# Performance work log

Hardware: AMD Instinct MI355X
Metric: run time of the kernel (lower is better)

Reference implementation:

```python
import jax, jax.numpy as jnp
import numpy as np

KL_W = 1.0
RECON_W = 1.0
TEMP_W = 0.1


def setup_inputs() -> dict:
    key = jax.random.key(0)
    ks = jax.random.split(key, 6)
    B, S, N, D = 4, 10, 2048, 128
    return {
        "pred_points": jax.random.normal(ks[0], (B, S, N, 3), jnp.float32),
        "target_points": jax.random.normal(ks[1], (B, S, N, 3), jnp.float32),
        "prior_mean": jax.random.normal(ks[2], (B, S, D), jnp.float32),
        "prior_log_var": jax.random.normal(ks[3], (B, S, D), jnp.float32),
        "posterior_mean": jax.random.normal(ks[4], (B, S, D), jnp.float32),
        "posterior_log_var": jax.random.normal(ks[5], (B, S, D), jnp.float32),
    }


def _chamfer(pred, tgt):
    # pred, tgt: [B, S, N, 3]; scan over time to keep only one [B,N,N] tile live
    B, S = pred.shape[0], pred.shape[1]

    def step(acc, pt):
        p, g = pt  # each [B, N, 3]
        diff = p[:, :, None, :] - g[:, None, :, :]            # [B, N, N, 3]
        d = jnp.sqrt(jnp.sum(diff * diff, axis=-1))           # [B, N, N]
        cd = jnp.mean(jnp.min(d, axis=2), axis=1) + jnp.mean(jnp.min(d, axis=1), axis=1)
        return acc + cd, None

    init = jnp.zeros((B,), pred.dtype)
    total, _ = jax.lax.scan(step, init,
                            (jnp.swapaxes(pred, 0, 1), jnp.swapaxes(tgt, 0, 1)))
    return jnp.mean(total) / S  # reduction='mean'


def _kl(prior_mean, prior_log_var, post_mean, post_log_var):
    kl = 0.5 * jnp.sum(
        prior_log_var - post_log_var
        + (jnp.exp(post_log_var) + (post_mean - prior_mean) ** 2) / jnp.exp(prior_log_var)
        - 1.0,
        axis=-1,
    )
    return jnp.mean(kl)


def _temporal(pred):
    diff = pred[:, 1:] - pred[:, :-1]                         # [B, S-1, N, 3]
    return jnp.mean(jnp.sqrt(jnp.sum(diff * diff, axis=-1)))


def reference(pred_points, target_points, prior_mean, prior_log_var,
              posterior_mean, posterior_log_var):
    recon = _chamfer(pred_points, target_points)
    kl = _kl(prior_mean, prior_log_var, posterior_mean, posterior_log_var)
    temporal = _temporal(pred_points)
    uncertainty = jnp.asarray(0.0, pred_points.dtype)
    total = RECON_W * recon + KL_W * kl + TEMP_W * temporal + 0.1 * uncertainty
    return (total, recon, kl, temporal, uncertainty)
```

## Files before the change

kernel.cpp:

```cpp
#include <hip/hip_runtime.h>
#include <hip/hip_bf16.h>
#include <math.h>

constexpr int B = 4, S = 10, N = 2048, D = 128;

constexpr int THREADS = 256;
constexpr int GHALF   = 1024;
constexpr int QBLK    = 256;
constexpr int QW      = 64;
constexpr int GT      = GHALF / 16;
constexpr int CHAM_BLOCKS = B * S * 2 * 2 * (N / QBLK);
constexpr int TOTQ    = B * S * 2 * N;
constexpr int TEMP_ELEMS = B * (S - 1) * N;
constexpr int TEMP_BLOCKS = 16;
constexpr int TEMP_PER_BLOCK = TEMP_ELEMS / TEMP_BLOCKS;
constexpr int KL_ELEMS = B * S * D;
constexpr int K2_BLOCKS = TOTQ / THREADS;
constexpr int K2_GRID   = K2_BLOCKS + TEMP_BLOCKS + 1;

constexpr size_t WS_SMAX  = 0;
constexpr size_t WS_CHSUM = (size_t)2 * TOTQ;
constexpr size_t WS_TPART = WS_CHSUM + K2_BLOCKS;
constexpr size_t WS_KL    = WS_TPART + TEMP_BLOCKS;

typedef __attribute__((ext_vector_type(8))) short bf16x8;
typedef __attribute__((ext_vector_type(4))) float f32x4;

__device__ __forceinline__ unsigned short f2bf(float f) {
    unsigned int b = __float_as_uint(f);
    b += 0x7FFFu + ((b >> 16) & 1u);
    return (unsigned short)(b >> 16);
}
__device__ __forceinline__ float bf2f(unsigned short h) {
    return __uint_as_float(((unsigned int)h) << 16);
}

__device__ __forceinline__ float block_sum(float v, float* red) {
    #pragma unroll
    for (int off = 32; off > 0; off >>= 1)
        v += __shfl_down(v, off, 64);
    const int wid = threadIdx.x >> 6;
    if ((threadIdx.x & 63) == 0) red[wid] = v;
    __syncthreads();
    return red[0] + red[1] + red[2] + red[3];
}

__global__ __launch_bounds__(256) void k1_kernel(
        const float* __restrict__ pred, const float* __restrict__ tgt,
        float* __restrict__ ws) {
    __shared__ alignas(16) unsigned short ghm[GT][16][8];
    __shared__ alignas(16) unsigned short glm[GT][16][8];
    __shared__ alignas(16) unsigned short zbuf[8];

    const int bid = blockIdx.x;
    const int tid = threadIdx.x;
    const int qg  = bid & 7;
    const int gh  = (bid >> 3) & 1;
    const int dir = (bid >> 4) & 1;
    const int bs  = bid >> 5;
    const float* qb  = (dir ? tgt : pred) + (size_t)bs * N * 3;
    const float* dbp = (dir ? pred : tgt) + (size_t)bs * N * 3;

    if (tid < 8) zbuf[tid] = 0;

    #pragma unroll
    for (int k = 0; k < 4; ++k) {
        const int p  = tid + 256 * k;
        const int gp = gh * GHALF + p;
        const float x = dbp[3 * gp + 0];
        const float y = dbp[3 * gp + 1];
        const float z = dbp[3 * gp + 2];
        const unsigned short hx = f2bf(x), hy = f2bf(y), hz = f2bf(z);
        const unsigned short lx = f2bf(x - bf2f(hx));
        const unsigned short ly = f2bf(y - bf2f(hy));
        const unsigned short lz = f2bf(z - bf2f(hz));
        const float m  = -0.5f * (x * x + y * y + z * z);
        const unsigned short mh = f2bf(m);
        const float m1 = m - bf2f(mh);
        const unsigned short ml = f2bf(m1);
        const unsigned short m3 = f2bf(m1 - bf2f(ml));
        bf16x8 gv, lv;
        gv[0] = (short)hx; gv[1] = (short)hy; gv[2] = (short)hz;
        gv[3] = (short)hx; gv[4] = (short)hy; gv[5] = (short)hz;
        gv[6] = (short)mh; gv[7] = (short)ml;
        lv[0] = (short)lx; lv[1] = (short)ly; lv[2] = (short)lz;
        lv[3] = (short)m3; lv[4] = 0; lv[5] = 0; lv[6] = 0; lv[7] = 0;
        *(bf16x8*)&ghm[p >> 4][p & 15][0] = gv;
        *(bf16x8*)&glm[p >> 4][p & 15][0] = lv;
    }

    const int lane = tid & 63, wid = tid >> 6;
    const int hi = lane >> 4, r = lane & 15;
    const int qwave = qg * QBLK + wid * QW;
    const short ONE = (short)0x3F80;
    bf16x8 a[4];
    #pragma unroll
    for (int qi = 0; qi < 4; ++qi) {
        bf16x8 v = (bf16x8)0;
        if (hi < 2) {
            const int q = qwave + qi * 16 + r;
            const float x = qb[3 * q + 0], y = qb[3 * q + 1], z = qb[3 * q + 2];
            const unsigned short hx = f2bf(x), hy = f2bf(y), hz = f2bf(z);
            if (hi == 0) {
                v[0] = (short)hx; v[1] = (short)hy; v[2] = (short)hz;
                v[3] = (short)f2bf(x - bf2f(hx));
                v[4] = (short)f2bf(y - bf2f(hy));
                v[5] = (short)f2bf(z - bf2f(hz));
                v[6] = ONE; v[7] = 0;
            } else {
                v[0] = (short)hx; v[1] = (short)hy; v[2] = (short)hz;
                v[3] = ONE;
            }
        }
        a[qi] = v;
    }
    __syncthreads();

    const char* bbase = (hi == 0) ? (const char*)&ghm[0][r][0]
                      : (hi == 1) ? (const char*)&glm[0][r][0]
                      :             (const char*)&zbuf[0];
    const int bstride = (hi < 2) ? 256 : 0;

    f32x4 rmax[4];
    #pragma unroll
    for (int qi = 0; qi < 4; ++qi) rmax[qi] = (f32x4)(-1e30f);
    const f32x4 zero4 = (f32x4)0.0f;

    for (int tp = 0; tp < GT / 2; ++tp) {
        const bf16x8 b0 = *(const bf16x8*)(bbase + (2 * tp + 0) * bstride);
        const bf16x8 b1 = *(const bf16x8*)(bbase + (2 * tp + 1) * bstride);
        #pragma unroll
        for (int qi = 0; qi < 4; ++qi) {
            const f32x4 c0 = __builtin_amdgcn_mfma_f32_16x16x32_bf16(a[qi], b0, zero4, 0, 0, 0);
            const f32x4 c1 = __builtin_amdgcn_mfma_f32_16x16x32_bf16(a[qi], b1, zero4, 0, 0, 0);
            #pragma unroll
            for (int j = 0; j < 4; ++j)
                rmax[qi][j] = fmaxf(rmax[qi][j], fmaxf(c0[j], c1[j]));
        }
    }

    #pragma unroll
    for (int qi = 0; qi < 4; ++qi) {
        #pragma unroll
        for (int j = 0; j < 4; ++j) {
            float v = rmax[qi][j];
            v = fmaxf(v, __shfl_xor(v, 1, 64));
            v = fmaxf(v, __shfl_xor(v, 2, 64));
            v = fmaxf(v, __shfl_xor(v, 4, 64));
            v = fmaxf(v, __shfl_xor(v, 8, 64));
            rmax[qi][j] = v;
        }
    }
    if (r == 0) {
        float* base = ws + WS_SMAX + (size_t)gh * TOTQ
                    + (size_t)(bs * 2 + dir) * N + qwave;
        #pragma unroll
        for (int qi = 0; qi < 4; ++qi)
            #pragma unroll
            for (int j = 0; j < 4; ++j)
                base[qi * 16 + hi * 4 + j] = rmax[qi][j];
    }
}

__global__ __launch_bounds__(256) void k2_kernel(
        const float* __restrict__ pred, const float* __restrict__ tgt,
        const float* __restrict__ prior_mean, const float* __restrict__ prior_lv,
        const float* __restrict__ post_mean,  const float* __restrict__ post_lv,
        float* __restrict__ ws) {
    __shared__ float red[4];
    const int bid = blockIdx.x;
    const int tid = threadIdx.x;

    if (bid < K2_BLOCKS) {
        const int u = bid * THREADS + tid;
        const float s = fmaxf(ws[WS_SMAX + u], ws[WS_SMAX + TOTQ + u]);
        const int n   = u & (N - 1);
        const int bsd = u >> 11;
        const int dir = bsd & 1, bs = bsd >> 1;
        const float* q = (dir ? tgt : pred) + ((size_t)bs * N + n) * 3;
        const float x = q[0], y = q[1], z = q[2];
        const float pn = x * x + y * y + z * z;
        const float d = sqrtf(fmaxf(pn - 2.0f * s, 0.0f));
        const float tot = block_sum(d, red);
        if (tid == 0) ws[WS_CHSUM + bid] = tot;
    } else if (bid < K2_BLOCKS + TEMP_BLOCKS) {
        const int tb = bid - K2_BLOCKS;
        float s = 0.0f;
        for (int it = 0; it < TEMP_PER_BLOCK / THREADS; ++it) {
            const int i = tb * TEMP_PER_BLOCK + it * THREADS + tid;
            const int b = i / ((S - 1) * N);
            const int rr = i % ((S - 1) * N);
            const float* p0 = pred + (size_t)(b * S * N + rr) * 3;
            const float* p1 = p0 + (size_t)N * 3;
            const float dx = p1[0] - p0[0];
            const float dy = p1[1] - p0[1];
            const float dz = p1[2] - p0[2];
            s += sqrtf(dx * dx + dy * dy + dz * dz);
        }
        const float tot = block_sum(s, red);
        if (tid == 0) ws[WS_TPART + tb] = tot;
    } else {
        float s = 0.0f;
        for (int it = 0; it < KL_ELEMS / THREADS; ++it) {
            const int i = it * THREADS + tid;
            const float aa = prior_lv[i];
            const float bb = post_lv[i];
            const float dm = post_mean[i] - prior_mean[i];
            s += aa - bb + (expf(bb) + dm * dm) * expf(-aa) - 1.0f;
        }
        const float tot = block_sum(s, red);
        if (tid == 0) ws[WS_KL] = tot;
    }
}

__global__ __launch_bounds__(256) void k3_kernel(const float* __restrict__ ws,
                                                 float* __restrict__ out) {
    __shared__ float red[4];
    float s = 0.0f;
    for (int i = threadIdx.x; i < K2_BLOCKS; i += THREADS)
        s += ws[WS_CHSUM + i];
    const float tot = block_sum(s, red);
    if (threadIdx.x == 0) {
        float tsum = 0.0f;
        for (int i = 0; i < TEMP_BLOCKS; ++i) tsum += ws[WS_TPART + i];
        const float recon    = tot / (float)(B * S * N);
        const float kl       = 0.5f * ws[WS_KL] / (float)(B * S);
        const float temporal = tsum / (float)TEMP_ELEMS;
        out[0] = recon + kl + 0.1f * temporal;
        out[1] = recon;
        out[2] = kl;
        out[3] = temporal;
        out[4] = 0.0f;
    }
}

extern "C" void kernel_launch(void* const* d_in, const int* in_sizes, int n_in,
                              void* d_out, int out_size, void* d_ws, size_t ws_size,
                              hipStream_t stream) {
    const float* pred = (const float*)d_in[0];
    const float* tgt  = (const float*)d_in[1];
    const float* pm   = (const float*)d_in[2];
    const float* plv  = (const float*)d_in[3];
    const float* qm   = (const float*)d_in[4];
    const float* qlv  = (const float*)d_in[5];
    float* out = (float*)d_out;
    float* ws  = (float*)d_ws;

    k1_kernel<<<CHAM_BLOCKS, THREADS, 0, stream>>>(pred, tgt, ws);
    k2_kernel<<<K2_GRID, THREADS, 0, stream>>>(pred, tgt, pm, plv, qm, qlv, ws);
    k3_kernel<<<1, THREADS, 0, stream>>>(ws, out);
}
```

Measured before the change: 97.69 us.

## Use 32x32 MFMA over full gallery and fuse chamfer finalize with temporal/KL

Each chamfer block now holds the full 2048-point gallery in LDS, uses 512 threads, and runs a 32x32x16 bf16 MFMA so the gallery no longer has to be split in halves. The min-distance finalize, temporal term and KL term move into the same kernel. This removes one launch and the workspace round-trip of partial maxima. In exchange LDS use and accumulator register pressure grow and the grid has half as many blocks.

```diff
diff --git a/kernel.cpp b/kernel.cpp
--- a/kernel.cpp
+++ b/kernel.cpp
@@ -4,27 +4,23 @@
 
 constexpr int B = 4, S = 10, N = 2048, D = 128;
 
-constexpr int THREADS = 256;
-constexpr int GHALF   = 1024;
+constexpr int THREADS = 512;
 constexpr int QBLK    = 256;
-constexpr int QW      = 64;
-constexpr int GT      = GHALF / 16;
-constexpr int CHAM_BLOCKS = B * S * 2 * 2 * (N / QBLK);
-constexpr int TOTQ    = B * S * 2 * N;
+constexpr int NQG     = N / QBLK;
+constexpr int GT      = N / 32;
+constexpr int CHAM_BLOCKS = B * S * 2 * NQG;
 constexpr int TEMP_ELEMS = B * (S - 1) * N;
 constexpr int TEMP_BLOCKS = 16;
 constexpr int TEMP_PER_BLOCK = TEMP_ELEMS / TEMP_BLOCKS;
 constexpr int KL_ELEMS = B * S * D;
-constexpr int K2_BLOCKS = TOTQ / THREADS;
-constexpr int K2_GRID   = K2_BLOCKS + TEMP_BLOCKS + 1;
-
-constexpr size_t WS_SMAX  = 0;
-constexpr size_t WS_CHSUM = (size_t)2 * TOTQ;
-constexpr size_t WS_TPART = WS_CHSUM + K2_BLOCKS;
+constexpr int K1_GRID  = CHAM_BLOCKS + TEMP_BLOCKS + 1;
+
+constexpr size_t WS_CHSUM = 0;
+constexpr size_t WS_TPART = CHAM_BLOCKS;
 constexpr size_t WS_KL    = WS_TPART + TEMP_BLOCKS;
 
-typedef __attribute__((ext_vector_type(8))) short bf16x8;
-typedef __attribute__((ext_vector_type(4))) float f32x4;
+typedef __attribute__((ext_vector_type(8)))  short bf16x8;
+typedef __attribute__((ext_vector_type(16))) float f32x16;
 
 __device__ __forceinline__ unsigned short f2bf(float f) {
     unsigned int b = __float_as_uint(f);
@@ -42,149 +38,121 @@
     const int wid = threadIdx.x >> 6;
     if ((threadIdx.x & 63) == 0) red[wid] = v;
     __syncthreads();
-    return red[0] + red[1] + red[2] + red[3];
-}
-
-__global__ __launch_bounds__(256) void k1_kernel(
+    float s = 0.0f;
+    if (threadIdx.x == 0)
+        #pragma unroll
+        for (int w = 0; w < 8; ++w) s += red[w];
+    return s;
+}
+
+__global__ __launch_bounds__(512) void k1_kernel(
         const float* __restrict__ pred, const float* __restrict__ tgt,
+        const float* __restrict__ prior_mean, const float* __restrict__ prior_lv,
+        const float* __restrict__ post_mean,  const float* __restrict__ post_lv,
         float* __restrict__ ws) {
-    __shared__ alignas(16) unsigned short ghm[GT][16][8];
-    __shared__ alignas(16) unsigned short glm[GT][16][8];
-    __shared__ alignas(16) unsigned short zbuf[8];
+    __shared__ alignas(16) unsigned short bh[GT][32][8];
+    __shared__ alignas(16) unsigned short bl[GT][32][8];
+    __shared__ float sm[8][32];
+    __shared__ float red[8];
 
     const int bid = blockIdx.x;
     const int tid = threadIdx.x;
-    const int qg  = bid & 7;
-    const int gh  = (bid >> 3) & 1;
-    const int dir = (bid >> 4) & 1;
-    const int bs  = bid >> 5;
-    const float* qb  = (dir ? tgt : pred) + (size_t)bs * N * 3;
-    const float* dbp = (dir ? pred : tgt) + (size_t)bs * N * 3;
-
-    if (tid < 8) zbuf[tid] = 0;
-
-    #pragma unroll
-    for (int k = 0; k < 4; ++k) {
-        const int p  = tid + 256 * k;
-        const int gp = gh * GHALF + p;
-        const float x = dbp[3 * gp + 0];
-        const float y = dbp[3 * gp + 1];
-        const float z = dbp[3 * gp + 2];
-        const unsigned short hx = f2bf(x), hy = f2bf(y), hz = f2bf(z);
-        const unsigned short lx = f2bf(x - bf2f(hx));
-        const unsigned short ly = f2bf(y - bf2f(hy));
-        const unsigned short lz = f2bf(z - bf2f(hz));
-        const float m  = -0.5f * (x * x + y * y + z * z);
-        const unsigned short mh = f2bf(m);
-        const float m1 = m - bf2f(mh);
-        const unsigned short ml = f2bf(m1);
-        const unsigned short m3 = f2bf(m1 - bf2f(ml));
-        bf16x8 gv, lv;
-        gv[0] = (short)hx; gv[1] = (short)hy; gv[2] = (short)hz;
-        gv[3] = (short)hx; gv[4] = (short)hy; gv[5] = (short)hz;
-        gv[6] = (short)mh; gv[7] = (short)ml;
-        lv[0] = (short)lx; lv[1] = (short)ly; lv[2] = (short)lz;
-        lv[3] = (short)m3; lv[4] = 0; lv[5] = 0; lv[6] = 0; lv[7] = 0;
-        *(bf16x8*)&ghm[p >> 4][p & 15][0] = gv;
-        *(bf16x8*)&glm[p >> 4][p & 15][0] = lv;
-    }
-
-    const int lane = tid & 63, wid = tid >> 6;
-    const int hi = lane >> 4, r = lane & 15;
-    const int qwave = qg * QBLK + wid * QW;
-    const short ONE = (short)0x3F80;
-    bf16x8 a[4];
-    #pragma unroll
-    for (int qi = 0; qi < 4; ++qi) {
-        bf16x8 v = (bf16x8)0;
-        if (hi < 2) {
-            const int q = qwave + qi * 16 + r;
-            const float x = qb[3 * q + 0], y = qb[3 * q + 1], z = qb[3 * q + 2];
-            const unsigned short hx = f2bf(x), hy = f2bf(y), hz = f2bf(z);
-            if (hi == 0) {
-                v[0] = (short)hx; v[1] = (short)hy; v[2] = (short)hz;
-                v[3] = (short)f2bf(x - bf2f(hx));
-                v[4] = (short)f2bf(y - bf2f(hy));
-                v[5] = (short)f2bf(z - bf2f(hz));
-                v[6] = ONE; v[7] = 0;
-            } else {
-                v[0] = (short)hx; v[1] = (short)hy; v[2] = (short)hz;
-                v[3] = ONE;
-            }
-        }
-        a[qi] = v;
-    }
-    __syncthreads();
-
-    const char* bbase = (hi == 0) ? (const char*)&ghm[0][r][0]
-                      : (hi == 1) ? (const char*)&glm[0][r][0]
-                      :             (const char*)&zbuf[0];
-    const int bstride = (hi < 2) ? 256 : 0;
-
-    f32x4 rmax[4];
-    #pragma unroll
-    for (int qi = 0; qi < 4; ++qi) rmax[qi] = (f32x4)(-1e30f);
-    const f32x4 zero4 = (f32x4)0.0f;
-
-    for (int tp = 0; tp < GT / 2; ++tp) {
-        const bf16x8 b0 = *(const bf16x8*)(bbase + (2 * tp + 0) * bstride);
-        const bf16x8 b1 = *(const bf16x8*)(bbase + (2 * tp + 1) * bstride);
-        #pragma unroll
-        for (int qi = 0; qi < 4; ++qi) {
-            const f32x4 c0 = __builtin_amdgcn_mfma_f32_16x16x32_bf16(a[qi], b0, zero4, 0, 0, 0);
-            const f32x4 c1 = __builtin_amdgcn_mfma_f32_16x16x32_bf16(a[qi], b1, zero4, 0, 0, 0);
-            #pragma unroll
-            for (int j = 0; j < 4; ++j)
-                rmax[qi][j] = fmaxf(rmax[qi][j], fmaxf(c0[j], c1[j]));
-        }
-    }
-
-    #pragma unroll
-    for (int qi = 0; qi < 4; ++qi) {
+
+    if (bid < CHAM_BLOCKS) {
+        const int qg  = bid & (NQG - 1);
+        const int dir = (bid >> 3) & 1;
+        const int bs  = bid >> 4;
+        const float* qb  = (dir ? tgt : pred) + (size_t)bs * N * 3;
+        const float* dbp = (dir ? pred : tgt) + (size_t)bs * N * 3;
+
         #pragma unroll
         for (int j = 0; j < 4; ++j) {
-            float v = rmax[qi][j];
+            const int p = tid + 512 * j;
+            const float x = dbp[3 * p + 0];
+            const float y = dbp[3 * p + 1];
+            const float z = dbp[3 * p + 2];
+            const unsigned short hx = f2bf(x), hy = f2bf(y), hz = f2bf(z);
+            const unsigned short lx = f2bf(x - bf2f(hx));
+            const unsigned short ly = f2bf(y - bf2f(hy));
+            const unsigned short lz = f2bf(z - bf2f(hz));
+            const float m  = -0.5f * (x * x + y * y + z * z);
+            const unsigned short mh = f2bf(m);
+            const float m1 = m - bf2f(mh);
+            const unsigned short ml = f2bf(m1);
+            const unsigned short m3 = f2bf(m1 - bf2f(ml));
+            bf16x8 gv, lv;
+            gv[0] = (short)hx; gv[1] = (short)hy; gv[2] = (short)hz;
+            gv[3] = (short)hx; gv[4] = (short)hy; gv[5] = (short)hz;
+            gv[6] = (short)mh; gv[7] = (short)ml;
+            lv[0] = (short)lx; lv[1] = (short)ly; lv[2] = (short)lz;
+            lv[3] = (short)m3; lv[4] = 0; lv[5] = 0; lv[6] = 0; lv[7] = 0;
+            *(bf16x8*)&bh[p >> 5][p & 31][0] = gv;
+            *(bf16x8*)&bl[p >> 5][p & 31][0] = lv;
+        }
+
+        const int lane = tid & 63, wid = tid >> 6;
+        const int hi = lane >> 5, qr = lane & 31;
+        const int q = qg * QBLK + wid * 32 + qr;
+        const float qx = qb[3 * q + 0], qy = qb[3 * q + 1], qz = qb[3 * q + 2];
+        const float pn = fmaf(qx, qx, fmaf(qy, qy, qz * qz));
+        const short ONE = (short)0x3F80;
+        bf16x8 a;
+        {
+            const unsigned short hx = f2bf(qx), hy = f2bf(qy), hz = f2bf(qz);
+            if (hi == 0) {
+                a[0] = (short)hx; a[1] = (short)hy; a[2] = (short)hz;
+                a[3] = (short)f2bf(qx - bf2f(hx));
+                a[4] = (short)f2bf(qy - bf2f(hy));
+                a[5] = (short)f2bf(qz - bf2f(hz));
+                a[6] = ONE; a[7] = 0;
+            } else {
+                a[0] = (short)hx; a[1] = (short)hy; a[2] = (short)hz;
+                a[3] = ONE; a[4] = 0; a[5] = 0; a[6] = 0; a[7] = 0;
+            }
+        }
+        __syncthreads();
+
+        const char* bbase = (hi ? (const char*)bl : (const char*)bh)
+                          + (size_t)qr * 16;
+        const f32x16 zero16 = (f32x16)0.0f;
+        f32x16 rmax = (f32x16)(-1e30f);
+        #pragma unroll 2
+        for (int tp = 0; tp < GT / 2; ++tp) {
+            const bf16x8 b0 = *(const bf16x8*)(bbase + (size_t)(2 * tp + 0) * 512);
+            const bf16x8 b1 = *(const bf16x8*)(bbase + (size_t)(2 * tp + 1) * 512);
+            const f32x16 c0 = __builtin_amdgcn_mfma_f32_32x32x16_bf16(a, b0, zero16, 0, 0, 0);
+            const f32x16 c1 = __builtin_amdgcn_mfma_f32_32x32x16_bf16(a, b1, zero16, 0, 0, 0);
+            #pragma unroll
+            for (int j = 0; j < 16; ++j)
+                rmax[j] = fmaxf(fmaxf(rmax[j], c0[j]), c1[j]);
+        }
+
+        #pragma unroll
+        for (int j = 0; j < 16; ++j) {
+            float v = rmax[j];
             v = fmaxf(v, __shfl_xor(v, 1, 64));
             v = fmaxf(v, __shfl_xor(v, 2, 64));
             v = fmaxf(v, __shfl_xor(v, 4, 64));
             v = fmaxf(v, __shfl_xor(v, 8, 64));
-            rmax[qi][j] = v;
-        }
-    }
-    if (r == 0) {
-        float* base = ws + WS_SMAX + (size_t)gh * TOTQ
-                    + (size_t)(bs * 2 + dir) * N + qwave;
-        #pragma unroll
-        for (int qi = 0; qi < 4; ++qi)
+            v = fmaxf(v, __shfl_xor(v, 16, 64));
+            rmax[j] = v;
+        }
+        if (qr == 0) {
             #pragma unroll
-            for (int j = 0; j < 4; ++j)
-                base[qi * 16 + hi * 4 + j] = rmax[qi][j];
-    }
-}
-
-__global__ __launch_bounds__(256) void k2_kernel(
-        const float* __restrict__ pred, const float* __restrict__ tgt,
-        const float* __restrict__ prior_mean, const float* __restrict__ prior_lv,
-        const float* __restrict__ post_mean,  const float* __restrict__ post_lv,
-        float* __restrict__ ws) {
-    __shared__ float red[4];
-    const int bid = blockIdx.x;
-    const int tid = threadIdx.x;
-
-    if (bid < K2_BLOCKS) {
-        const int u = bid * THREADS + tid;
-        const float s = fmaxf(ws[WS_SMAX + u], ws[WS_SMAX + TOTQ + u]);
-        const int n   = u & (N - 1);
-        const int bsd = u >> 11;
-        const int dir = bsd & 1, bs = bsd >> 1;
-        const float* q = (dir ? tgt : pred) + ((size_t)bs * N + n) * 3;
-        const float x = q[0], y = q[1], z = q[2];
-        const float pn = x * x + y * y + z * z;
-        const float d = sqrtf(fmaxf(pn - 2.0f * s, 0.0f));
+            for (int j = 0; j < 16; ++j)
+                sm[wid][(j & 3) + 8 * (j >> 2) + 4 * hi] = rmax[j];
+        }
+        __syncthreads();
+
+        float d = 0.0f;
+        if (lane < 32) {
+            const float s = sm[wid][qr];
+            d = sqrtf(fmaxf(pn - 2.0f * s, 0.0f));
+        }
         const float tot = block_sum(d, red);
         if (tid == 0) ws[WS_CHSUM + bid] = tot;
-    } else if (bid < K2_BLOCKS + TEMP_BLOCKS) {
-        const int tb = bid - K2_BLOCKS;
+    } else if (bid < CHAM_BLOCKS + TEMP_BLOCKS) {
+        const int tb = bid - CHAM_BLOCKS;
         float s = 0.0f;
         for (int it = 0; it < TEMP_PER_BLOCK / THREADS; ++it) {
             const int i = tb * TEMP_PER_BLOCK + it * THREADS + tid;
@@ -213,11 +181,11 @@
     }
 }
 
-__global__ __launch_bounds__(256) void k3_kernel(const float* __restrict__ ws,
+__global__ __launch_bounds__(512) void k3_kernel(const float* __restrict__ ws,
                                                  float* __restrict__ out) {
-    __shared__ float red[4];
+    __shared__ float red[8];
     float s = 0.0f;
-    for (int i = threadIdx.x; i < K2_BLOCKS; i += THREADS)
+    for (int i = threadIdx.x; i < CHAM_BLOCKS; i += THREADS)
         s += ws[WS_CHSUM + i];
     const float tot = block_sum(s, red);
     if (threadIdx.x == 0) {
@@ -246,7 +214,6 @@
     float* out = (float*)d_out;
     float* ws  = (float*)d_ws;
 
-    k1_kernel<<<CHAM_BLOCKS, THREADS, 0, stream>>>(pred, tgt, ws);
-    k2_kernel<<<K2_GRID, THREADS, 0, stream>>>(pred, tgt, pm, plv, qm, qlv, ws);
+    k1_kernel<<<K1_GRID, THREADS, 0, stream>>>(pred, tgt, pm, plv, qm, qlv, ws);
     k3_kernel<<<1, THREADS, 0, stream>>>(ws, out);
 }
```

After: 82.62 us. -15.4%, faster.
